# Optimization experiments

Hardware: AMD Instinct MI355X
Metric: run time of the kernel (lower is better)

Reference implementation:

```python
import jax, jax.numpy as jnp
import numpy as np

COMMITMENT_COST = 0.25

def setup_inputs() -> dict:
    key = jax.random.key(0)
    k1, k2 = jax.random.split(key)
    inputs = jax.random.normal(k1, (32, 64, 64, 64), dtype=jnp.float32)  # NCHW, C == embedding_dim
    num_embeddings, embedding_dim = 512, 64
    # nn.Embedding weight init: uniform(-1/num_embeddings, 1/num_embeddings)
    weight = jax.random.uniform(k2, (num_embeddings, embedding_dim), dtype=jnp.float32,
                                minval=-1.0 / num_embeddings, maxval=1.0 / num_embeddings)
    return {"inputs": inputs, "weight": weight}

def reference(inputs, weight):
    B, C, H, W = inputs.shape
    K, D = weight.shape
    # permute to NHWC then flatten tokens: [B*H*W, D]
    flat = jnp.transpose(inputs, (0, 2, 3, 1)).reshape(-1, D)
    # squared L2 distances to each codebook vector: [N, K]
    distances = (jnp.sum(flat * flat, axis=1, keepdims=True)
                 - 2.0 * flat @ weight.T
                 + jnp.sum(weight * weight, axis=1))
    encoding_indices = jnp.argmin(distances, axis=1)  # [N]
    # direct gather instead of one-hot matmul (same math)
    # NOTE: original code views flat (NHWC-ordered) rows back into the NCHW
    # input shape WITHOUT inverse-permuting -- replicated faithfully here.
    quantized = weight[encoding_indices].reshape(inputs.shape)
    e_latent_loss = jnp.mean((jax.lax.stop_gradient(quantized) - inputs) ** 2)
    q_latent_loss = jnp.mean((quantized - jax.lax.stop_gradient(inputs)) ** 2)
    loss = q_latent_loss + COMMITMENT_COST * e_latent_loss
    # straight-through estimator
    quantized_st = inputs + jax.lax.stop_gradient(quantized - inputs)
    # perplexity via index counts (equivalent to mean of one-hot encodings)
    N = flat.shape[0]
    counts = jnp.zeros((K,), dtype=flat.dtype).at[encoding_indices].add(1.0)
    avg_probs = counts / N
    perplexity = jnp.exp(-jnp.sum(avg_probs * jnp.log(avg_probs + 1e-10)))
    return quantized_st, loss, perplexity
```

## Files before the change

kernel.cpp:

```cpp
#include <hip/hip_runtime.h>
#include <math.h>


#define NTOK 131072
#define KCODES 512
#define HW 4096
#define CHW 262144
#define NELEM 8388608

typedef __attribute__((ext_vector_type(8))) short short8;
typedef __attribute__((ext_vector_type(4))) float f32x4;
typedef __attribute__((ext_vector_type(4))) unsigned short u16x4;

static __device__ __forceinline__ unsigned short f2bf(float f) {
    unsigned u = __float_as_uint(f);
    unsigned r = u + 0x7FFFu + ((u >> 16) & 1u);
    return (unsigned short)(r >> 16);
}

__global__ __launch_bounds__(512, 8) void vq_main(const float* __restrict__ in,
                                                  const float* __restrict__ w,
                                                  float* __restrict__ out,
                                                  unsigned short* __restrict__ pcounts,
                                                  double* __restrict__ ssep,
                                                  float* __restrict__ counts,
                                                  double* __restrict__ sse_acc,
                                                  const int amode) {
    __shared__ __align__(16) unsigned short wh[256 * 64];
    __shared__ float wsqp[KCODES];
    __shared__ int idxbuf[256];
    __shared__ int hist[KCODES];
    __shared__ double sred[8];

    const int tid = threadIdx.x;
    const int lane = tid & 63, wv = tid >> 6;
    const int col = lane & 15, quad = lane >> 4;
    const int ntok0 = blockIdx.x * 256;

    wsqp[tid] = 1.25f;
    hist[tid] = 0;
    __syncthreads();

    const float* gbase = in + (ntok0 >> 12) * CHW + (ntok0 & 4095) + wv * 32 + col;
    short8 ah[2][2];
    float xsq = 0.f;
#pragma unroll
    for (int it = 0; it < 8; ++it) {
        const int sub = it >> 2, c = (it >> 1) & 1, j0 = (it & 1) * 4;
        const float* gp = gbase + sub * 16 + (c * 32 + quad * 8 + j0) * HW;
        const float x0 = gp[0 * HW], x1 = gp[1 * HW], x2 = gp[2 * HW], x3 = gp[3 * HW];

        if (it < 4) {
            const int g = it * 512 + tid;
            const int cc = g & 15, qd = (g >> 4) & 3, ch = (g >> 6) & 1, tt = g >> 7;
            const int code = tt * 16 + cc;
            const float4* src = (const float4*)(w + code * 64 + ch * 32 + qd * 8);
            const float4 v0 = src[0], v1 = src[1];
            short8 hv;
            hv[0] = (short)f2bf(v0.x); hv[1] = (short)f2bf(v0.y);
            hv[2] = (short)f2bf(v0.z); hv[3] = (short)f2bf(v0.w);
            hv[4] = (short)f2bf(v1.x); hv[5] = (short)f2bf(v1.y);
            hv[6] = (short)f2bf(v1.z); hv[7] = (short)f2bf(v1.w);
            *(short8*)(wh + g * 8) = hv;
            float ws2 = v0.x * v0.x;
            ws2 = fmaf(v0.y, v0.y, ws2); ws2 = fmaf(v0.z, v0.z, ws2);
            ws2 = fmaf(v0.w, v0.w, ws2); ws2 = fmaf(v1.x, v1.x, ws2);
            ws2 = fmaf(v1.y, v1.y, ws2); ws2 = fmaf(v1.z, v1.z, ws2);
            ws2 = fmaf(v1.w, v1.w, ws2);
            atomicAdd(&wsqp[code], ws2);
        }

        ah[sub][c][j0 + 0] = (short)f2bf(-2.0f * x0);
        ah[sub][c][j0 + 1] = (short)f2bf(-2.0f * x1);
        ah[sub][c][j0 + 2] = (short)f2bf(-2.0f * x2);
        ah[sub][c][j0 + 3] = (short)f2bf(-2.0f * x3);
        xsq = fmaf(x0, x0, xsq); xsq = fmaf(x1, x1, xsq);
        xsq = fmaf(x2, x2, xsq); xsq = fmaf(x3, x3, xsq);
    }
    __syncthreads();

    unsigned runkey[2][4];
#pragma unroll
    for (int sub = 0; sub < 2; ++sub)
#pragma unroll
        for (int r = 0; r < 4; ++r) runkey[sub][r] = 0xFFFFFFFFu;

#pragma unroll 1
    for (int t = 0; t < 16; ++t) {
        const unsigned short* ph = wh + t * 1024 + quad * 128 + col * 8;
        const short8 b0 = *(const short8*)ph;
        const short8 b1 = *(const short8*)(ph + 512);
        const int code = t * 16 + col;
        const float seed = wsqp[code];
#pragma unroll
        for (int sub = 0; sub < 2; ++sub) {
            f32x4 acc = {seed, seed, seed, seed};
            acc = __builtin_amdgcn_mfma_f32_16x16x32_bf16(ah[sub][0], b0, acc, 0, 0, 0);
            acc = __builtin_amdgcn_mfma_f32_16x16x32_bf16(ah[sub][1], b1, acc, 0, 0, 0);
#pragma unroll
            for (int r = 0; r < 4; ++r) {
                const unsigned key = (__float_as_uint(acc[r]) << 9) | code;
                runkey[sub][r] = key < runkey[sub][r] ? key : runkey[sub][r];
            }
        }
    }
    __syncthreads();

#pragma unroll
    for (int it = 0; it < 4; ++it) {
        const int g = it * 512 + tid;
        const int cc = g & 15, qd = (g >> 4) & 3, ch = (g >> 6) & 1, tt = g >> 7;
        const int code = 256 + tt * 16 + cc;
        const float4* src = (const float4*)(w + code * 64 + ch * 32 + qd * 8);
        const float4 v0 = src[0], v1 = src[1];
        short8 hv;
        hv[0] = (short)f2bf(v0.x); hv[1] = (short)f2bf(v0.y);
        hv[2] = (short)f2bf(v0.z); hv[3] = (short)f2bf(v0.w);
        hv[4] = (short)f2bf(v1.x); hv[5] = (short)f2bf(v1.y);
        hv[6] = (short)f2bf(v1.z); hv[7] = (short)f2bf(v1.w);
        *(short8*)(wh + g * 8) = hv;
        float ws2 = v0.x * v0.x;
        ws2 = fmaf(v0.y, v0.y, ws2); ws2 = fmaf(v0.z, v0.z, ws2);
        ws2 = fmaf(v0.w, v0.w, ws2); ws2 = fmaf(v1.x, v1.x, ws2);
        ws2 = fmaf(v1.y, v1.y, ws2); ws2 = fmaf(v1.z, v1.z, ws2);
        ws2 = fmaf(v1.w, v1.w, ws2);
        atomicAdd(&wsqp[code], ws2);
    }
    __syncthreads();

#pragma unroll 1
    for (int t = 0; t < 16; ++t) {
        const unsigned short* ph = wh + t * 1024 + quad * 128 + col * 8;
        const short8 b0 = *(const short8*)ph;
        const short8 b1 = *(const short8*)(ph + 512);
        const int code = 256 + t * 16 + col;
        const float seed = wsqp[code];
#pragma unroll
        for (int sub = 0; sub < 2; ++sub) {
            f32x4 acc = {seed, seed, seed, seed};
            acc = __builtin_amdgcn_mfma_f32_16x16x32_bf16(ah[sub][0], b0, acc, 0, 0, 0);
            acc = __builtin_amdgcn_mfma_f32_16x16x32_bf16(ah[sub][1], b1, acc, 0, 0, 0);
#pragma unroll
            for (int r = 0; r < 4; ++r) {
                const unsigned key = (__float_as_uint(acc[r]) << 9) | code;
                runkey[sub][r] = key < runkey[sub][r] ? key : runkey[sub][r];
            }
        }
    }

#pragma unroll
    for (int s = 1; s < 16; s <<= 1)
#pragma unroll
        for (int sub = 0; sub < 2; ++sub)
#pragma unroll
            for (int r = 0; r < 4; ++r) {
                const unsigned o = __shfl_xor(runkey[sub][r], s, 64);
                runkey[sub][r] = o < runkey[sub][r] ? o : runkey[sub][r];
            }

    float dsum = 0.f;
    if (col == 0) {
#pragma unroll
        for (int sub = 0; sub < 2; ++sub)
#pragma unroll
            for (int r = 0; r < 4; ++r) {
                const unsigned key = runkey[sub][r];
                idxbuf[wv * 32 + sub * 16 + quad * 4 + r] = (int)(key & 511u);
                dsum += __uint_as_float((key >> 9) | 0x3F800000u) - 1.25f;
            }
    }
    float contrib = xsq + dsum;
#pragma unroll
    for (int off = 32; off > 0; off >>= 1) contrib += __shfl_down(contrib, off, 64);
    if (lane == 0) sred[wv] = (double)contrib;

    if (lane < 32) atomicAdd(&hist[idxbuf[wv * 32 + lane]], 1);

#pragma unroll
    for (int p = 0; p < 2; ++p) {
        const int tl = p * 16 + (lane >> 2), q = lane & 3;
        const int n = ntok0 + wv * 32 + tl;
        const int bidx = idxbuf[wv * 32 + tl];
        const float4* wr = (const float4*)(w + bidx * 64 + q * 16);
        float4* op = (float4*)(out + n * 64 + q * 16);
#pragma unroll
        for (int i = 0; i < 4; ++i) op[i] = wr[i];
    }
    __syncthreads();

    if (!amode) {
        pcounts[(blockIdx.x << 9) + tid] = (unsigned short)hist[tid];
        if (tid == 0) {
            double s = sred[0];
#pragma unroll
            for (int i = 1; i < 8; ++i) s += sred[i];
            ssep[blockIdx.x] = s;
        }
    } else {
        const int h = hist[tid];
        if (h) atomicAdd(&counts[tid], (float)h);
        if (tid == 0) {
            double s = sred[0];
#pragma unroll
            for (int i = 1; i < 8; ++i) s += sred[i];
            atomicAdd(sse_acc, s);
        }
    }
}

__global__ __launch_bounds__(512) void vq_final_p(const unsigned short* __restrict__ pcounts,
                                                  const double* __restrict__ ssep,
                                                  float* __restrict__ out) {
    __shared__ float part[4][512];
    __shared__ double red[512];
    __shared__ double sred[512];
    const int t = threadIdx.x;
    const int q = t >> 7, c4 = (t & 127) << 2;

    const u16x4* base = (const u16x4*)pcounts + (q << 14) + (c4 >> 2);
    float4 s = {0.f, 0.f, 0.f, 0.f};
#pragma unroll 16
    for (int b = 0; b < 128; ++b) {
        const u16x4 v = base[b << 7];
        s.x += (float)v[0]; s.y += (float)v[1];
        s.z += (float)v[2]; s.w += (float)v[3];
    }
    *(float4*)&part[q][c4] = s;
    sred[t] = ssep[t];
    __syncthreads();

    const float cnt = part[0][t] + part[1][t] + part[2][t] + part[3][t];
    const double p = (double)cnt / (double)NTOK;
    red[t] = p * log(p + 1e-10);
    __syncthreads();
#pragma unroll
    for (int st = 256; st > 0; st >>= 1) {
        if (t < st) { red[t] += red[t + st]; sred[t] += sred[t + st]; }
        __syncthreads();
    }
    if (t == 0) {
        out[NELEM] = (float)((sred[0] / (double)NELEM) * 1.25);
        out[NELEM + 1] = (float)exp(-red[0]);
    }
}

__global__ __launch_bounds__(512) void vq_final_a(const float* __restrict__ counts,
                                                  const double* __restrict__ sse_acc,
                                                  float* __restrict__ out) {
    __shared__ double red[512];
    const int k = threadIdx.x;
    const double p = (double)counts[k] / (double)NTOK;
    red[k] = p * log(p + 1e-10);
    __syncthreads();
#pragma unroll
    for (int st = 256; st > 0; st >>= 1) {
        if (k < st) red[k] += red[k + st];
        __syncthreads();
    }
    if (k == 0) {
        out[NELEM] = (float)((*sse_acc / (double)NELEM) * 1.25);
        out[NELEM + 1] = (float)exp(-red[0]);
    }
}

extern "C" void kernel_launch(void* const* d_in, const int* in_sizes, int n_in,
                              void* d_out, int out_size, void* d_ws, size_t ws_size,
                              hipStream_t stream) {
    const float* in = (const float*)d_in[0];
    const float* w = (const float*)d_in[1];
    float* out = (float*)d_out;
    char* ws = (char*)d_ws;

    const size_t SS = (size_t)512 * 512 * 2;
    const size_t need = SS + 512 * 8;
    if (ws_size >= need) {
        unsigned short* pcounts = (unsigned short*)ws;
        double* ssep = (double*)(ws + SS);
        vq_main<<<512, 512, 0, stream>>>(in, w, out, pcounts, ssep,
                                         nullptr, nullptr, 0);
        vq_final_p<<<1, 512, 0, stream>>>(pcounts, ssep, out);
    } else {
        float* counts = (float*)ws;
        double* sse_acc = (double*)(ws + 2048);
        (void)hipMemsetAsync(ws, 0, 2056, stream);
        vq_main<<<512, 512, 0, stream>>>(in, w, out, nullptr, nullptr,
                                         counts, sse_acc, 1);
        vq_final_a<<<1, 512, 0, stream>>>(counts, sse_acc, out);
    }
}
```

Before: 116.5 us.

## Fuse final reduction into main kernel via last-block flag spin-wait

Drops the separate vq_final_p launch. Each block now publishes its per-code counts (widened to 32-bit) and its partial SSE with agent-scope atomic stores, then sets a release flag. Block 0 spins until all 512 flags are set, then does the histogram sum, the entropy/perplexity reduction and the loss write. This saves a kernel launch and its serialization gap. In exchange it relies on all blocks being co-resident, doubles the partial-count traffic, and never resets the flags, so later calls can see stale flags and read partial counts before they are rewritten.

Measured after the change: 137.5 us. +18.0%, slower.

```diff
diff --git a/kernel.cpp b/kernel.cpp
--- a/kernel.cpp
+++ b/kernel.cpp
@@ -7,10 +7,10 @@
 #define HW 4096
 #define CHW 262144
 #define NELEM 8388608
+#define FLAG_MAGIC 0x5AFE0512u
 
 typedef __attribute__((ext_vector_type(8))) short short8;
 typedef __attribute__((ext_vector_type(4))) float f32x4;
-typedef __attribute__((ext_vector_type(4))) unsigned short u16x4;
 
 static __device__ __forceinline__ unsigned short f2bf(float f) {
     unsigned u = __float_as_uint(f);
@@ -21,8 +21,9 @@
 __global__ __launch_bounds__(512, 8) void vq_main(const float* __restrict__ in,
                                                   const float* __restrict__ w,
                                                   float* __restrict__ out,
-                                                  unsigned short* __restrict__ pcounts,
-                                                  double* __restrict__ ssep,
+                                                  unsigned* __restrict__ pcounts,
+                                                  unsigned long long* __restrict__ ssep,
+                                                  unsigned* __restrict__ flags,
                                                   float* __restrict__ counts,
                                                   double* __restrict__ sse_acc,
                                                   const int amode) {
@@ -189,12 +190,63 @@
     __syncthreads();
 
     if (!amode) {
-        pcounts[(blockIdx.x << 9) + tid] = (unsigned short)hist[tid];
+        __hip_atomic_store(&pcounts[(blockIdx.x << 9) + tid], (unsigned)hist[tid],
+                           __ATOMIC_RELAXED, __HIP_MEMORY_SCOPE_AGENT);
         if (tid == 0) {
             double s = sred[0];
 #pragma unroll
             for (int i = 1; i < 8; ++i) s += sred[i];
-            ssep[blockIdx.x] = s;
+            __hip_atomic_store(&ssep[blockIdx.x],
+                               (unsigned long long)__double_as_longlong(s),
+                               __ATOMIC_RELAXED, __HIP_MEMORY_SCOPE_AGENT);
+        }
+        __syncthreads();
+        if (tid == 0)
+            __hip_atomic_store(&flags[blockIdx.x], FLAG_MAGIC,
+                               __ATOMIC_RELEASE, __HIP_MEMORY_SCOPE_AGENT);
+
+        if (blockIdx.x == 0) {
+            for (;;) {
+                const unsigned f = __hip_atomic_load(&flags[tid], __ATOMIC_RELAXED,
+                                                     __HIP_MEMORY_SCOPE_AGENT);
+                if (__syncthreads_and(f == FLAG_MAGIC)) break;
+                __builtin_amdgcn_s_sleep(16);
+            }
+            unsigned c0 = 0, c1 = 0, c2 = 0, c3 = 0;
+            const unsigned* pc = pcounts + tid;
+#pragma unroll 2
+            for (int b = 0; b < 512; b += 16) {
+                unsigned v[16];
+#pragma unroll
+                for (int j = 0; j < 16; ++j)
+                    v[j] = __hip_atomic_load(pc + ((b + j) << 9), __ATOMIC_RELAXED,
+                                             __HIP_MEMORY_SCOPE_AGENT);
+#pragma unroll
+                for (int j = 0; j < 16; j += 4) {
+                    c0 += v[j]; c1 += v[j + 1]; c2 += v[j + 2]; c3 += v[j + 3];
+                }
+            }
+            const float cnt = (float)(c0 + c1 + c2 + c3);
+            double* const dred = (double*)wh;
+            double* const dsred = dred + KCODES;
+            const double p = (double)cnt / (double)NTOK;
+            dred[tid] = p * log(p + 1e-10);
+            dsred[tid] = __longlong_as_double(
+                (long long)__hip_atomic_load(&ssep[tid], __ATOMIC_RELAXED,
+                                             __HIP_MEMORY_SCOPE_AGENT));
+            __syncthreads();
+#pragma unroll
+            for (int st = 256; st > 0; st >>= 1) {
+                if (tid < st) {
+                    dred[tid] += dred[tid + st];
+                    dsred[tid] += dsred[tid + st];
+                }
+                __syncthreads();
+            }
+            if (tid == 0) {
+                out[NELEM] = (float)((dsred[0] / (double)NELEM) * 1.25);
+                out[NELEM + 1] = (float)exp(-dred[0]);
+            }
         }
     } else {
         const int h = hist[tid];
@@ -205,42 +257,6 @@
             for (int i = 1; i < 8; ++i) s += sred[i];
             atomicAdd(sse_acc, s);
         }
-    }
-}
-
-__global__ __launch_bounds__(512) void vq_final_p(const unsigned short* __restrict__ pcounts,
-                                                  const double* __restrict__ ssep,
-                                                  float* __restrict__ out) {
-    __shared__ float part[4][512];
-    __shared__ double red[512];
-    __shared__ double sred[512];
-    const int t = threadIdx.x;
-    const int q = t >> 7, c4 = (t & 127) << 2;
-
-    const u16x4* base = (const u16x4*)pcounts + (q << 14) + (c4 >> 2);
-    float4 s = {0.f, 0.f, 0.f, 0.f};
-#pragma unroll 16
-    for (int b = 0; b < 128; ++b) {
-        const u16x4 v = base[b << 7];
-        s.x += (float)v[0]; s.y += (float)v[1];
-        s.z += (float)v[2]; s.w += (float)v[3];
-    }
-    *(float4*)&part[q][c4] = s;
-    sred[t] = ssep[t];
-    __syncthreads();
-
-    const float cnt = part[0][t] + part[1][t] + part[2][t] + part[3][t];
-    const double p = (double)cnt / (double)NTOK;
-    red[t] = p * log(p + 1e-10);
-    __syncthreads();
-#pragma unroll
-    for (int st = 256; st > 0; st >>= 1) {
-        if (t < st) { red[t] += red[t + st]; sred[t] += sred[t + st]; }
-        __syncthreads();
-    }
-    if (t == 0) {
-        out[NELEM] = (float)((sred[0] / (double)NELEM) * 1.25);
-        out[NELEM + 1] = (float)exp(-red[0]);
     }
 }
 
@@ -271,19 +287,21 @@
     float* out = (float*)d_out;
     char* ws = (char*)d_ws;
 
-    const size_t SS = (size_t)512 * 512 * 2;
-    const size_t need = SS + 512 * 8;
+    const size_t PC = 0;
+    const size_t SS = (size_t)512 * 512 * 4;
+    const size_t FL = SS + 512 * 8;
+    const size_t need = FL + 512 * 4;
     if (ws_size >= need) {
-        unsigned short* pcounts = (unsigned short*)ws;
-        double* ssep = (double*)(ws + SS);
-        vq_main<<<512, 512, 0, stream>>>(in, w, out, pcounts, ssep,
+        unsigned* pcounts = (unsigned*)(ws + PC);
+        unsigned long long* ssep = (unsigned long long*)(ws + SS);
+        unsigned* flags = (unsigned*)(ws + FL);
+        vq_main<<<512, 512, 0, stream>>>(in, w, out, pcounts, ssep, flags,
                                          nullptr, nullptr, 0);
-        vq_final_p<<<1, 512, 0, stream>>>(pcounts, ssep, out);
     } else {
         float* counts = (float*)ws;
         double* sse_acc = (double*)(ws + 2048);
         (void)hipMemsetAsync(ws, 0, 2056, stream);
-        vq_main<<<512, 512, 0, stream>>>(in, w, out, nullptr, nullptr,
+        vq_main<<<512, 512, 0, stream>>>(in, w, out, nullptr, nullptr, nullptr,
                                          counts, sse_acc, 1);
         vq_final_a<<<1, 512, 0, stream>>>(counts, sse_acc, out);
     }
```
